# Kernel tuning notes

Measured on AMD Instinct MI355X. Metric: run time of the kernel, lower is better.

The kernel has to match this reference:

```python
import jax, jax.numpy as jnp
import numpy as np

M, K, N = 8192, 4096, 4096
DIV = 1.0 / (127.0 * 127.0)


def setup_inputs() -> dict:
    key = jax.random.key(0)
    k1, k2, k3, k4, k5 = jax.random.split(key, 5)
    x = jax.random.randint(k1, (M, K), -127, 128, dtype=jnp.int8)
    weight_int8 = jax.random.randint(k2, (N, K), -127, 128, dtype=jnp.int8)
    scale_x = jnp.abs(jax.random.normal(k3, (M,), dtype=jnp.float32)) * 0.01
    scale_w = jnp.abs(jax.random.normal(k4, (N,), dtype=jnp.float32)) * 0.01
    bias = (jax.random.normal(k5, (N,), dtype=jnp.float32) * 0.01).astype(jnp.float16)
    return {"x": x, "scale_x": scale_x, "weight_int8": weight_int8,
            "scale_w": scale_w, "bias": bias}


def reference(x, scale_x, weight_int8, scale_w, bias):
    # int8 GEMM with int32 accumulation: [M,K] @ [K,N]
    acc = jax.lax.dot_general(
        x, weight_int8.T,
        dimension_numbers=(((1,), (0,)), ((), ())),
        preferred_element_type=jnp.int32,
    ).astype(jnp.float32)
    # fused rowwise/colwise dequant + bias, cast to fp16
    out = acc * DIV * scale_x[:, None] * scale_w[None, :] + bias.astype(jnp.float32)[None, :]
    return out.astype(jnp.float16)
```

## Files before the change

kernel.cpp:

```cpp
#include <hip/hip_runtime.h>
#include <hip/hip_fp16.h>
#include <cstdint>
#include <cstddef>

#define M_DIM 8192
#define N_DIM 4096
#define K_DIM 4096

typedef int v4i __attribute__((ext_vector_type(4)));

__global__ __launch_bounds__(256) void pack_i32_to_i8(const int* __restrict__ src,
                                                      uint32_t* __restrict__ dst,
                                                      int n4) {
    int i = blockIdx.x * 256 + threadIdx.x;
    if (i >= n4) return;
    int4 a = ((const int4*)src)[i];
#if __has_builtin(__builtin_amdgcn_perm)
    uint32_t lo = __builtin_amdgcn_perm((uint32_t)a.y, (uint32_t)a.x, 0x0400);
    uint32_t hi = __builtin_amdgcn_perm((uint32_t)a.w, (uint32_t)a.z, 0x0400);
    dst[i] = __builtin_amdgcn_perm(hi, lo, 0x05040100);
#else
    dst[i] = (uint32_t)(a.x & 0xff) | ((uint32_t)(a.y & 0xff) << 8) |
             ((uint32_t)(a.z & 0xff) << 16) | ((uint32_t)a.w << 24);
#endif
}

__device__ __forceinline__ void gload_lds16(const int8_t* g, int8_t* l) {
    __builtin_amdgcn_global_load_lds(
        (const __attribute__((address_space(1))) void*)g,
        (__attribute__((address_space(3))) void*)l, 16, 0, 0);
}

__global__ __launch_bounds__(256) void gemm_i8_dq(const int8_t* __restrict__ A,
                                                  const int8_t* __restrict__ W,
                                                  const float* __restrict__ sx,
                                                  const float* __restrict__ sw,
                                                  const float* __restrict__ bias,
                                                  float* __restrict__ out) {
    __shared__ int8_t sA[128 * 64];
    __shared__ int8_t sB[128 * 64];

    const int t    = threadIdx.x;
    const int lane = t & 63;
    const int w    = t >> 6;
    const int wm   = w >> 1;
    const int wn   = w & 1;

    const int flat = blockIdx.y * 32 + blockIdx.x;
    const int xcd  = flat & 7;
    const int idx  = flat >> 3;
    const int bn   = (xcd & 3) * 8 + (idx & 7);
    const int bm   = (xcd >> 2) * 32 + (idx >> 3);

    const int srow   = t >> 2;
    const int rot    = (srow >> 1) & 3;
    const int gchunk = ((t & 3) + rot) & 3;
    const int scol   = gchunk * 16;
    const int8_t* gA0 = A + (size_t)(bm * 128 + srow) * K_DIM + scol;
    const int8_t* gA1 = A + (size_t)(bm * 128 + 64 + srow) * K_DIM + scol;
    const int8_t* gB0 = W + (size_t)(bn * 128 + srow) * K_DIM + scol;
    const int8_t* gB1 = W + (size_t)(bn * 128 + 64 + srow) * K_DIM + scol;
    int8_t* lA0 = &sA[t * 16];
    int8_t* lA1 = &sA[4096 + t * 16];
    int8_t* lB0 = &sB[t * 16];
    int8_t* lB1 = &sB[4096 + t * 16];

    const int rho  = lane & 15;
    const int p16  = (((lane >> 4) - (rho >> 1)) & 3) * 16;
    const int aoff = (wm * 64 + rho) * 64 + p16;
    const int boff = (wn * 64 + rho) * 64 + p16;

    v4i acc[4][4];
    const v4i vzero = {0, 0, 0, 0};
#pragma unroll
    for (int mi = 0; mi < 4; mi++)
#pragma unroll
        for (int ni = 0; ni < 4; ni++) acc[mi][ni] = vzero;

    for (int kt = 0; kt < K_DIM; kt += 64) {
        __syncthreads();
        gload_lds16(gA0 + kt, lA0);
        gload_lds16(gA1 + kt, lA1);
        gload_lds16(gB0 + kt, lB0);
        gload_lds16(gB1 + kt, lB1);
        __syncthreads();

        v4i af[4], bf[4];
#pragma unroll
        for (int i = 0; i < 4; i++) {
            af[i] = *(const v4i*)(&sA[aoff + i * 1024]);
            bf[i] = *(const v4i*)(&sB[boff + i * 1024]);
        }
#pragma unroll
        for (int mi = 0; mi < 4; mi++)
#pragma unroll
            for (int ni = 0; ni < 4; ni++)
                acc[mi][ni] = __builtin_amdgcn_mfma_i32_16x16x64_i8(
                    af[mi], bf[ni], acc[mi][ni], 0, 0, 0);
    }

    const float DIVF = (float)(1.0 / (127.0 * 127.0));
    const int col0 = bn * 128 + wn * 64 + (lane & 15);
    const int row0 = bm * 128 + wm * 64 + (lane >> 4) * 4;

    float swv[4], bv[4];
#pragma unroll
    for (int ni = 0; ni < 4; ni++) {
        swv[ni] = sw[col0 + ni * 16];
        bv[ni]  = bias[col0 + ni * 16];
    }

#pragma unroll
    for (int mi = 0; mi < 4; mi++) {
#pragma unroll
        for (int r = 0; r < 4; r++) {
            const int row = row0 + mi * 16 + r;
            const float xs = sx[row];
#pragma unroll
            for (int ni = 0; ni < 4; ni++) {
                float v = __fmul_rn((float)acc[mi][ni][r], DIVF);
                v = __fmul_rn(v, xs);
                v = __fmul_rn(v, swv[ni]);
                v = __fadd_rn(v, bv[ni]);
                out[(size_t)row * N_DIM + col0 + ni * 16] = __half2float(__float2half(v));
            }
        }
    }
}

extern "C" void kernel_launch(void* const* d_in, const int* in_sizes, int n_in,
                              void* d_out, int out_size, void* d_ws, size_t ws_size,
                              hipStream_t stream) {
    const int*   x_i32 = (const int*)d_in[0];
    const float* sx    = (const float*)d_in[1];
    const int*   w_i32 = (const int*)d_in[2];
    const float* sw    = (const float*)d_in[3];
    const float* bias  = (const float*)d_in[4];
    float* out = (float*)d_out;

    uint8_t* xb = (uint8_t*)d_ws;
    uint8_t* wb = (uint8_t*)d_ws + (size_t)M_DIM * K_DIM;

    const int nx4 = (M_DIM * K_DIM) / 4;
    const int nw4 = (N_DIM * K_DIM) / 4;
    pack_i32_to_i8<<<(nx4 + 255) / 256, 256, 0, stream>>>(x_i32, (uint32_t*)xb, nx4);
    pack_i32_to_i8<<<(nw4 + 255) / 256, 256, 0, stream>>>(w_i32, (uint32_t*)wb, nw4);

    dim3 grid(N_DIM / 128, M_DIM / 128);
    gemm_i8_dq<<<grid, 256, 0, stream>>>((const int8_t*)xb, (const int8_t*)wb,
                                         sx, sw, bias, out);
}
```

Before: 422.0 us.

## Enlarge GEMM tile to 256x256 with four-stage LDS prefetch pipeline and merge pack kernels

The int8 GEMM moves from 128x128 tiles with 256 threads to 256x256 tiles with 512 threads (8 waves, each computing 128x64). It replaces the load-then-compute loop with a four-buffer LDS ring that prefetches three K-tiles ahead. Global-to-LDS loads are interleaved between two MFMA phases using explicit barriers, vmcnt waits and setprio. This aims to hide global memory latency and raise arithmetic intensity per byte loaded. The two int32-to-int8 pack launches are also merged into one. In exchange, the kernel uses 128KB of LDS and many more accumulator registers, which limits it to one block per CU.

```diff
diff --git a/kernel.cpp b/kernel.cpp
--- a/kernel.cpp
+++ b/kernel.cpp
@@ -9,19 +9,26 @@
 
 typedef int v4i __attribute__((ext_vector_type(4)));
 
-__global__ __launch_bounds__(256) void pack_i32_to_i8(const int* __restrict__ src,
-                                                      uint32_t* __restrict__ dst,
-                                                      int n4) {
+__global__ __launch_bounds__(256) void pack_i32_to_i8(const int* __restrict__ srcX,
+                                                      uint32_t* __restrict__ dstX,
+                                                      const int* __restrict__ srcW,
+                                                      uint32_t* __restrict__ dstW,
+                                                      int nx4, int ntot) {
     int i = blockIdx.x * 256 + threadIdx.x;
-    if (i >= n4) return;
-    int4 a = ((const int4*)src)[i];
+    if (i >= ntot) return;
+    const int* s;
+    uint32_t*  d;
+    int j;
+    if (i < nx4) { s = srcX; d = dstX; j = i; }
+    else         { s = srcW; d = dstW; j = i - nx4; }
+    int4 a = ((const int4*)s)[j];
 #if __has_builtin(__builtin_amdgcn_perm)
     uint32_t lo = __builtin_amdgcn_perm((uint32_t)a.y, (uint32_t)a.x, 0x0400);
     uint32_t hi = __builtin_amdgcn_perm((uint32_t)a.w, (uint32_t)a.z, 0x0400);
-    dst[i] = __builtin_amdgcn_perm(hi, lo, 0x05040100);
+    d[j] = __builtin_amdgcn_perm(hi, lo, 0x05040100);
 #else
-    dst[i] = (uint32_t)(a.x & 0xff) | ((uint32_t)(a.y & 0xff) << 8) |
-             ((uint32_t)(a.z & 0xff) << 16) | ((uint32_t)a.w << 24);
+    d[j] = (uint32_t)(a.x & 0xff) | ((uint32_t)(a.y & 0xff) << 8) |
+           ((uint32_t)(a.z & 0xff) << 16) | ((uint32_t)a.w << 24);
 #endif
 }
 
@@ -31,77 +38,120 @@
         (__attribute__((address_space(3))) void*)l, 16, 0, 0);
 }
 
-__global__ __launch_bounds__(256) void gemm_i8_dq(const int8_t* __restrict__ A,
-                                                  const int8_t* __restrict__ W,
-                                                  const float* __restrict__ sx,
-                                                  const float* __restrict__ sw,
-                                                  const float* __restrict__ bias,
-                                                  float* __restrict__ out) {
-    __shared__ int8_t sA[128 * 64];
-    __shared__ int8_t sB[128 * 64];
+
+#define VMW(n) asm volatile("s_waitcnt vmcnt(" #n ")" ::: "memory")
+
+#define PH_MFMA(MBASE)                                                        \
+    __builtin_amdgcn_s_setprio(1);                                            \
+    _Pragma("unroll")                                                         \
+    for (int mi = 0; mi < 4; ++mi) {                                          \
+        _Pragma("unroll")                                                     \
+        for (int ni = 0; ni < 4; ++ni)                                        \
+            acc[(MBASE) + mi][ni] = __builtin_amdgcn_mfma_i32_16x16x64_i8(    \
+                af[mi], bf[ni], acc[(MBASE) + mi][ni], 0, 0, 0);              \
+    }                                                                         \
+    __builtin_amdgcn_s_setprio(0);
+
+#define KTILE(KT, DO_STAGE, VMSTMT)                                           \
+    do {                                                                      \
+        int8_t* bufA = lds + ((KT) & 3) * 32768;                              \
+        int8_t* bufB = bufA + 16384;                                          \
+        v4i af[4], bf[4];                                                     \
+                  \
+        _Pragma("unroll")                                                     \
+        for (int i = 0; i < 4; ++i) {                                         \
+            af[i] = *(const v4i*)(bufA + aoff + i * 1024);                    \
+            bf[i] = *(const v4i*)(bufB + boff + i * 1024);                    \
+        }                                                                     \
+        if (DO_STAGE) {                                                       \
+            int8_t* sAb = lds + (((KT) + 3) & 3) * 32768;                     \
+            gload_lds16(gA0 + ((KT) + 3) * 64, sAb + ldsoff);                 \
+            gload_lds16(gA1 + ((KT) + 3) * 64, sAb + ldsoff + 8192);          \
+        }                                                                     \
+        __builtin_amdgcn_s_barrier();                                         \
+        asm volatile("s_waitcnt lgkmcnt(0)" ::: "memory");                    \
+        __builtin_amdgcn_sched_barrier(0);                                    \
+        PH_MFMA(0)                                                            \
+        __builtin_amdgcn_s_barrier();                                         \
+                  \
+        _Pragma("unroll")                                                     \
+        for (int i = 0; i < 4; ++i)                                           \
+            af[i] = *(const v4i*)(bufA + aoff + 4096 + i * 1024);             \
+        if (DO_STAGE) {                                                       \
+            int8_t* sBb = lds + (((KT) + 3) & 3) * 32768 + 16384;             \
+            gload_lds16(gB0 + ((KT) + 3) * 64, sBb + ldsoff);                 \
+            gload_lds16(gB1 + ((KT) + 3) * 64, sBb + ldsoff + 8192);          \
+        }                                                                     \
+        __builtin_amdgcn_s_barrier();                                         \
+        asm volatile("s_waitcnt lgkmcnt(0)" ::: "memory");                    \
+        __builtin_amdgcn_sched_barrier(0);                                    \
+        PH_MFMA(4)                                                            \
+        VMSTMT;                                                               \
+        __builtin_amdgcn_s_barrier();                                         \
+    } while (0)
+
+__global__ __launch_bounds__(512, 2) void gemm_i8_dq(const int8_t* __restrict__ A,
+                                                     const int8_t* __restrict__ W,
+                                                     const float* __restrict__ sx,
+                                                     const float* __restrict__ sw,
+                                                     const float* __restrict__ bias,
+                                                     float* __restrict__ out) {
+    __shared__ __attribute__((aligned(16))) int8_t lds[131072];
 
     const int t    = threadIdx.x;
     const int lane = t & 63;
     const int w    = t >> 6;
-    const int wm   = w >> 1;
-    const int wn   = w & 1;
-
-    const int flat = blockIdx.y * 32 + blockIdx.x;
+    const int wm   = w >> 2;
+    const int wn   = w & 3;
+
+    const int flat = blockIdx.y * 16 + blockIdx.x;
     const int xcd  = flat & 7;
     const int idx  = flat >> 3;
-    const int bn   = (xcd & 3) * 8 + (idx & 7);
-    const int bm   = (xcd >> 2) * 32 + (idx >> 3);
+    const int bm   = (xcd >> 1) * 8 + (idx & 7);
+    const int bn   = (xcd & 1) * 8 + (idx >> 3);
 
     const int srow   = t >> 2;
     const int rot    = (srow >> 1) & 3;
     const int gchunk = ((t & 3) + rot) & 3;
     const int scol   = gchunk * 16;
-    const int8_t* gA0 = A + (size_t)(bm * 128 + srow) * K_DIM + scol;
-    const int8_t* gA1 = A + (size_t)(bm * 128 + 64 + srow) * K_DIM + scol;
-    const int8_t* gB0 = W + (size_t)(bn * 128 + srow) * K_DIM + scol;
-    const int8_t* gB1 = W + (size_t)(bn * 128 + 64 + srow) * K_DIM + scol;
-    int8_t* lA0 = &sA[t * 16];
-    int8_t* lA1 = &sA[4096 + t * 16];
-    int8_t* lB0 = &sB[t * 16];
-    int8_t* lB1 = &sB[4096 + t * 16];
+    const int8_t* gA0 = A + (size_t)(bm * 256 + srow) * K_DIM + scol;
+    const int8_t* gA1 = gA0 + (size_t)128 * K_DIM;
+    const int8_t* gB0 = W + (size_t)(bn * 256 + srow) * K_DIM + scol;
+    const int8_t* gB1 = gB0 + (size_t)128 * K_DIM;
+    const int ldsoff = t * 16;
 
     const int rho  = lane & 15;
     const int p16  = (((lane >> 4) - (rho >> 1)) & 3) * 16;
-    const int aoff = (wm * 64 + rho) * 64 + p16;
+    const int aoff = (wm * 128 + rho) * 64 + p16;
     const int boff = (wn * 64 + rho) * 64 + p16;
 
-    v4i acc[4][4];
+    v4i acc[8][4];
     const v4i vzero = {0, 0, 0, 0};
 #pragma unroll
-    for (int mi = 0; mi < 4; mi++)
+    for (int mi = 0; mi < 8; mi++)
 #pragma unroll
         for (int ni = 0; ni < 4; ni++) acc[mi][ni] = vzero;
 
-    for (int kt = 0; kt < K_DIM; kt += 64) {
-        __syncthreads();
-        gload_lds16(gA0 + kt, lA0);
-        gload_lds16(gA1 + kt, lA1);
-        gload_lds16(gB0 + kt, lB0);
-        gload_lds16(gB1 + kt, lB1);
-        __syncthreads();
-
-        v4i af[4], bf[4];
-#pragma unroll
-        for (int i = 0; i < 4; i++) {
-            af[i] = *(const v4i*)(&sA[aoff + i * 1024]);
-            bf[i] = *(const v4i*)(&sB[boff + i * 1024]);
-        }
-#pragma unroll
-        for (int mi = 0; mi < 4; mi++)
-#pragma unroll
-            for (int ni = 0; ni < 4; ni++)
-                acc[mi][ni] = __builtin_amdgcn_mfma_i32_16x16x64_i8(
-                    af[mi], bf[ni], acc[mi][ni], 0, 0, 0);
+#pragma unroll
+    for (int pt = 0; pt < 3; ++pt) {
+        int8_t* bufA = lds + pt * 32768;
+        int8_t* bufB = bufA + 16384;
+        gload_lds16(gA0 + pt * 64, bufA + ldsoff);
+        gload_lds16(gA1 + pt * 64, bufA + ldsoff + 8192);
+        gload_lds16(gB0 + pt * 64, bufB + ldsoff);
+        gload_lds16(gB1 + pt * 64, bufB + ldsoff + 8192);
     }
+    VMW(8);
+    __builtin_amdgcn_s_barrier();
+
+    for (int kt = 0; kt < 61; ++kt) KTILE(kt, true, VMW(8));
+    KTILE(61, false, VMW(4));
+    KTILE(62, false, VMW(0));
+    KTILE(63, false, ((void)0));
 
     const float DIVF = (float)(1.0 / (127.0 * 127.0));
-    const int col0 = bn * 128 + wn * 64 + (lane & 15);
-    const int row0 = bm * 128 + wm * 64 + (lane >> 4) * 4;
+    const int col0 = bn * 256 + wn * 64 + (lane & 15);
+    const int row0 = bm * 256 + wm * 128 + (lane >> 4) * 4;
 
     float swv[4], bv[4];
 #pragma unroll
@@ -111,7 +161,7 @@
     }
 
 #pragma unroll
-    for (int mi = 0; mi < 4; mi++) {
+    for (int mi = 0; mi < 8; mi++) {
 #pragma unroll
         for (int r = 0; r < 4; r++) {
             const int row = row0 + mi * 16 + r;
@@ -141,12 +191,13 @@
     uint8_t* xb = (uint8_t*)d_ws;
     uint8_t* wb = (uint8_t*)d_ws + (size_t)M_DIM * K_DIM;
 
-    const int nx4 = (M_DIM * K_DIM) / 4;
-    const int nw4 = (N_DIM * K_DIM) / 4;
-    pack_i32_to_i8<<<(nx4 + 255) / 256, 256, 0, stream>>>(x_i32, (uint32_t*)xb, nx4);
-    pack_i32_to_i8<<<(nw4 + 255) / 256, 256, 0, stream>>>(w_i32, (uint32_t*)wb, nw4);
-
-    dim3 grid(N_DIM / 128, M_DIM / 128);
-    gemm_i8_dq<<<grid, 256, 0, stream>>>((const int8_t*)xb, (const int8_t*)wb,
+    const int nx4  = (M_DIM * K_DIM) / 4;
+    const int nw4  = (N_DIM * K_DIM) / 4;
+    const int ntot = nx4 + nw4;
+    pack_i32_to_i8<<<(ntot + 255) / 256, 256, 0, stream>>>(
+        x_i32, (uint32_t*)xb, w_i32, (uint32_t*)wb, nx4, ntot);
+
+    dim3 grid(N_DIM / 256, M_DIM / 256);
+    gemm_i8_dq<<<grid, 512, 0, stream>>>((const int8_t*)xb, (const int8_t*)wb,
                                          sx, sw, bias, out);
 }
```

Result: faster. 392.9 us (-6.9%).
